# Performance work log

Measured on AMD Instinct MI355X. Metric: run time of the kernel, lower is better.

Reference implementation:

```python
import jax, jax.numpy as jnp
import numpy as np

D_MODEL = 2048
N_HEADS = 16
HEAD_DIM = 128
WINDOW = 512
ROPE_BASE = 10000.0
B, N = 2, 2048
INNER = N_HEADS * HEAD_DIM


def setup_inputs() -> dict:
    key = jax.random.key(0)
    k1, k2, k3 = jax.random.split(key, 3)
    x = jax.random.normal(k1, (B, N, D_MODEL), dtype=jnp.float32)
    # torch nn.Linear stores weight as [out_features, in_features]
    w_qkv = jax.random.normal(k2, (3 * INNER, D_MODEL), dtype=jnp.float32) / np.sqrt(D_MODEL)
    w_o = jax.random.normal(k3, (D_MODEL, INNER), dtype=jnp.float32) / np.sqrt(INNER)
    return {"x": x, "w_qkv": w_qkv, "w_o": w_o}


def _rotate_half(t):
    t1, t2 = jnp.split(t, 2, axis=-1)
    return jnp.concatenate([-t2, t1], axis=-1)


def _rope(q, k, offset=0):
    # q, k: [B, H, N, D]; GPT-NeoX half-split rotary embedding
    D = q.shape[-1]
    inv_freq = 1.0 / (ROPE_BASE ** (jnp.arange(0, D, 2, dtype=jnp.float32) / D))
    pos = jnp.arange(q.shape[2], dtype=jnp.float32) + offset
    ang = pos[:, None] * inv_freq[None, :]                 # [N, D/2]
    cos = jnp.concatenate([jnp.cos(ang), jnp.cos(ang)], axis=-1)  # [N, D]
    sin = jnp.concatenate([jnp.sin(ang), jnp.sin(ang)], axis=-1)
    q_r = q * cos + _rotate_half(q) * sin
    k_r = k * cos + _rotate_half(k) * sin
    return q_r, k_r


def reference(x, w_qkv, w_o):
    Bq, Nq, _ = x.shape
    # QKV projection (no bias)
    qkv = jnp.einsum('bnd,ed->bne', x, w_qkv)              # [B, N, 3*INNER]
    q, k, v = jnp.split(qkv, 3, axis=-1)
    def to_heads(t):
        return t.reshape(Bq, Nq, N_HEADS, HEAD_DIM).transpose(0, 2, 1, 3)  # [B,H,N,D]
    q, k, v = to_heads(q), to_heads(k), to_heads(v)
    q, k = _rope(q, k, offset=0)
    # sliding-window causal mask: valid key j for query i iff (i - WINDOW) < j <= i
    i = jnp.arange(Nq)[:, None]
    j = jnp.arange(Nq)[None, :]
    valid = (j > i - WINDOW) & (j <= i)                    # [N, N]
    scale = 1.0 / np.sqrt(HEAD_DIM)
    scores = jnp.einsum('bhnd,bhkd->bhnk', q, k) * scale   # [B,H,N,N]
    scores = jnp.where(valid[None, None], scores, -jnp.inf)
    att = jax.nn.softmax(scores, axis=-1)
    out = jnp.einsum('bhnk,bhkd->bhnd', att, v)
    out = out.transpose(0, 2, 1, 3).reshape(Bq, Nq, INNER)
    y = jnp.einsum('bni,di->bnd', out, w_o)
    return y
```

## Files before the change

kernel.cpp:

```cpp
#include <hip/hip_runtime.h>
#include <hip/hip_bf16.h>
#include <cstdint>

typedef __bf16 bf16x8 __attribute__((ext_vector_type(8)));
typedef float floatx4 __attribute__((ext_vector_type(4)));

__device__ __forceinline__ void gl2lds16(const void* g, void* l) {
  __builtin_amdgcn_global_load_lds(
      (const __attribute__((address_space(1))) unsigned int*)g,
      (__attribute__((address_space(3))) unsigned int*)(uintptr_t)l,
      16, 0, 0);
}

__global__ __launch_bounds__(256)
void cvt_kernel(const float* __restrict__ in, __hip_bfloat16* __restrict__ out, int n) {
  int i = (blockIdx.x * 256 + threadIdx.x) * 4;
  if (i >= n) return;
  const float4 v = *(const float4*)(in + i);
  out[i + 0] = __float2bfloat16(v.x);
  out[i + 1] = __float2bfloat16(v.y);
  out[i + 2] = __float2bfloat16(v.z);
  out[i + 3] = __float2bfloat16(v.w);
}

__global__ __launch_bounds__(256)
void gemm_bt(const __hip_bfloat16* __restrict__ A, const __hip_bfloat16* __restrict__ Bm,
             void* __restrict__ Cp, int M, int Nc, int K, int c_fp32)
{
  __shared__ __hip_bfloat16 As[128 * 32];
  __shared__ __hip_bfloat16 Bs[128 * 32];
  const int tid = threadIdx.x;
  const int lane = tid & 63, wave = tid >> 6;
  const int wm = (wave & 1) * 64, wn = (wave >> 1) * 64;
  const int m0 = blockIdx.x * 128, n0 = blockIdx.y * 128;
  const int lrow = lane & 15, lk = (lane >> 4) * 8;
  floatx4 acc[4][4] = {};
  const int c0 = tid, c1 = tid + 256;
  const int r0 = c0 >> 2, o0 = (c0 & 3) * 8;
  const int r1 = c1 >> 2, o1 = (c1 & 3) * 8;
  for (int kt = 0; kt < K; kt += 32) {
    __syncthreads();
    gl2lds16(A + (size_t)(m0 + r0) * K + kt + o0, &As[c0 * 8]);
    gl2lds16(A + (size_t)(m0 + r1) * K + kt + o1, &As[c1 * 8]);
    gl2lds16(Bm + (size_t)(n0 + r0) * K + kt + o0, &Bs[c0 * 8]);
    gl2lds16(Bm + (size_t)(n0 + r1) * K + kt + o1, &Bs[c1 * 8]);
    __syncthreads();
    bf16x8 af[4], bfr[4];
#pragma unroll
    for (int t = 0; t < 4; t++) af[t] = *(const bf16x8*)&As[(wm + t * 16 + lrow) * 32 + lk];
#pragma unroll
    for (int t = 0; t < 4; t++) bfr[t] = *(const bf16x8*)&Bs[(wn + t * 16 + lrow) * 32 + lk];
#pragma unroll
    for (int mt = 0; mt < 4; mt++)
#pragma unroll
      for (int nt = 0; nt < 4; nt++)
        acc[mt][nt] = __builtin_amdgcn_mfma_f32_16x16x32_bf16(af[mt], bfr[nt], acc[mt][nt], 0, 0, 0);
  }
  const int lq4 = (lane >> 4) * 4;
#pragma unroll
  for (int mt = 0; mt < 4; mt++)
#pragma unroll
    for (int nt = 0; nt < 4; nt++)
#pragma unroll
      for (int r = 0; r < 4; r++) {
        const int m = m0 + wm + mt * 16 + lq4 + r;
        const int n = n0 + wn + nt * 16 + lrow;
        const float v = acc[mt][nt][r];
        if (c_fp32) ((float*)Cp)[(size_t)m * Nc + n] = v;
        else ((__hip_bfloat16*)Cp)[(size_t)m * Nc + n] = __float2bfloat16(v);
      }
}

__global__ __launch_bounds__(256)
void gemm_qkv_fused(const __hip_bfloat16* __restrict__ A,
                    const __hip_bfloat16* __restrict__ W,
                    __hip_bfloat16* __restrict__ Qr,
                    __hip_bfloat16* __restrict__ Kr,
                    __hip_bfloat16* __restrict__ Vt)
{
  __shared__ alignas(16) char smem[16640];
  __shared__ float invf[64];
  __hip_bfloat16* As = (__hip_bfloat16*)smem;
  __hip_bfloat16* Bs = As + 128 * 32;
  __hip_bfloat16* Cs = (__hip_bfloat16*)smem;
  const int tid = threadIdx.x;
  if (tid < 64) invf[tid] = __expf(-(float)tid * 0.14391156831212787f);
  const int lane = tid & 63, wave = tid >> 6;
  const int wm = (wave & 1) * 64, wn = (wave >> 1) * 64;
  const int m0 = blockIdx.x * 128, n0 = blockIdx.y * 128;
  const int K = 2048;
  const int lrow = lane & 15, lk = (lane >> 4) * 8;
  floatx4 acc[4][4] = {};
  const int c0 = tid, c1 = tid + 256;
  const int r0 = c0 >> 2, o0 = (c0 & 3) * 8;
  const int r1 = c1 >> 2, o1 = (c1 & 3) * 8;
  for (int kt = 0; kt < K; kt += 32) {
    __syncthreads();
    gl2lds16(A + (size_t)(m0 + r0) * K + kt + o0, &As[c0 * 8]);
    gl2lds16(A + (size_t)(m0 + r1) * K + kt + o1, &As[c1 * 8]);
    gl2lds16(W + (size_t)(n0 + r0) * K + kt + o0, &Bs[c0 * 8]);
    gl2lds16(W + (size_t)(n0 + r1) * K + kt + o1, &Bs[c1 * 8]);
    __syncthreads();
    bf16x8 af[4], bfr[4];
#pragma unroll
    for (int t = 0; t < 4; t++) af[t] = *(const bf16x8*)&As[(wm + t * 16 + lrow) * 32 + lk];
#pragma unroll
    for (int t = 0; t < 4; t++) bfr[t] = *(const bf16x8*)&Bs[(wn + t * 16 + lrow) * 32 + lk];
#pragma unroll
    for (int mt = 0; mt < 4; mt++)
#pragma unroll
      for (int nt = 0; nt < 4; nt++)
        acc[mt][nt] = __builtin_amdgcn_mfma_f32_16x16x32_bf16(af[mt], bfr[nt], acc[mt][nt], 0, 0, 0);
  }
  const int lq4 = (lane >> 4) * 4;
  const int seg = n0 >> 11;
  const int h = (n0 & 2047) >> 7;
  const int b = m0 >> 11;
  const int bh = b * 16 + h;
  const int seq0 = m0 & 2047;
  const float qscale = (seg == 0) ? 0.08838834764831845f : 1.0f;
  for (int pass = 0; pass < 2; ++pass) {
    __syncthreads();
    if ((wave & 1) == pass) {
#pragma unroll
      for (int mt = 0; mt < 4; mt++)
#pragma unroll
        for (int nt = 0; nt < 4; nt++)
#pragma unroll
          for (int r = 0; r < 4; r++)
            Cs[(mt * 16 + lq4 + r) * 130 + wn + nt * 16 + lrow] =
                __float2bfloat16(acc[mt][nt][r]);
    }
    __syncthreads();
    if (seg < 2) {
      __hip_bfloat16* Out = seg ? Kr : Qr;
#pragma unroll
      for (int p = 0; p < 2; ++p) {
        const int row = (tid >> 3) + p * 32;
        const int oct = (tid & 7) * 8;
        const int m = m0 + pass * 64 + row;
        const float pos = (float)(m & 2047);
        alignas(16) __hip_bfloat16 lo[8], hi[8];
#pragma unroll
        for (int k2 = 0; k2 < 8; k2++) {
          const float ang = pos * invf[oct + k2];
          float sn, cs2;
          __sincosf(ang, &sn, &cs2);
          const float a  = __bfloat162float(Cs[row * 130 + oct + k2]);
          const float bb = __bfloat162float(Cs[row * 130 + oct + k2 + 64]);
          lo[k2] = __float2bfloat16((a * cs2 - bb * sn) * qscale);
          hi[k2] = __float2bfloat16((bb * cs2 + a * sn) * qscale);
        }
        const size_t ob = ((size_t)bh * 2048 + (size_t)(m & 2047)) * 128;
        *(bf16x8*)&Out[ob + oct]      = *(const bf16x8*)lo;
        *(bf16x8*)&Out[ob + oct + 64] = *(const bf16x8*)hi;
      }
    } else {
#pragma unroll
      for (int p = 0; p < 4; ++p) {
        const int d = (tid >> 3) + p * 32;
        const int s8 = (tid & 7) * 8;
        alignas(16) __hip_bfloat16 tmp[8];
#pragma unroll
        for (int k2 = 0; k2 < 8; k2++) tmp[k2] = Cs[(s8 + k2) * 130 + d];
        const size_t ob = ((size_t)bh * 128 + d) * 2048 + seq0 + pass * 64 + s8;
        *(bf16x8*)&Vt[ob] = *(const bf16x8*)tmp;
      }
    }
  }
}

__global__ __launch_bounds__(256)
void attn_swa(const __hip_bfloat16* __restrict__ Qr, const __hip_bfloat16* __restrict__ Kr,
              const __hip_bfloat16* __restrict__ Vt, __hip_bfloat16* __restrict__ Out)
{
  __shared__ __hip_bfloat16 Qs[64 * 128];
  __shared__ __hip_bfloat16 Ks[64 * 128];
  __shared__ __hip_bfloat16 Vs[128 * 64];
  __shared__ __hip_bfloat16 Pb[4][16 * 64];
  const int qt = blockIdx.x, bh = blockIdx.y;
  const int tid = threadIdx.x, lane = tid & 63, wave = tid >> 6;
  const int lrow = lane & 15, lk = (lane >> 4) * 8, lq4 = (lane >> 4) * 4;
  const int i0 = qt * 64;
  const float NEG_INF = -__builtin_inff();
  const __hip_bfloat16* Qh = Qr + (size_t)bh * 2048 * 128;
  const __hip_bfloat16* Kh = Kr + (size_t)bh * 2048 * 128;
  const __hip_bfloat16* Vh = Vt + (size_t)bh * 128 * 2048;
#pragma unroll
  for (int it = 0; it < 4; it++) {
    const int c = it * 256 + tid;
    gl2lds16(Qh + (size_t)(i0 + (c >> 4)) * 128 + (c & 15) * 8, &Qs[c * 8]);
  }
  floatx4 accO[8] = {};
  float m_i[4], l_i[4];
#pragma unroll
  for (int r = 0; r < 4; r++) { m_i[r] = NEG_INF; l_i[r] = 0.f; }
  const int lo = i0 - 511;
  const int jt_lo = (lo > 0 ? lo : 0) >> 6;
  const int jt_hi = i0 >> 6;
  const int imin = i0 + wave * 16;
  bf16x8 aq[4];
  for (int jt = jt_lo; jt <= jt_hi; jt++) {
    const int j0 = jt * 64;
    __syncthreads();
#pragma unroll
    for (int it = 0; it < 4; it++) {
      const int c = it * 256 + tid;
      gl2lds16(Kh + (size_t)(j0 + (c >> 4)) * 128 + (c & 15) * 8, &Ks[c * 8]);
      gl2lds16(Vh + (size_t)(c >> 3) * 2048 + j0 + (c & 7) * 8, &Vs[c * 8]);
    }
    __syncthreads();
    if (jt == jt_lo) {
#pragma unroll
      for (int ks = 0; ks < 4; ks++)
        aq[ks] = *(const bf16x8*)&Qs[(wave * 16 + lrow) * 128 + ks * 32 + lk];
    }
    floatx4 s[4] = {};
#pragma unroll
    for (int nt = 0; nt < 4; nt++)
#pragma unroll
      for (int ks = 0; ks < 4; ks++) {
        const bf16x8 bk = *(const bf16x8*)&Ks[(nt * 16 + lrow) * 128 + ks * 32 + lk];
        s[nt] = __builtin_amdgcn_mfma_f32_16x16x32_bf16(aq[ks], bk, s[nt], 0, 0, 0);
      }
    const bool full = (j0 + 63 <= imin) && (j0 >= imin + 15 - 511);
    float rmax[4];
#pragma unroll
    for (int r = 0; r < 4; r++) rmax[r] = NEG_INF;
    if (full) {
#pragma unroll
      for (int nt = 0; nt < 4; nt++)
#pragma unroll
        for (int r = 0; r < 4; r++) rmax[r] = fmaxf(rmax[r], s[nt][r]);
    } else {
#pragma unroll
      for (int nt = 0; nt < 4; nt++) {
        const int j = j0 + nt * 16 + lrow;
#pragma unroll
        for (int r = 0; r < 4; r++) {
          const int i = i0 + wave * 16 + lq4 + r;
          const float sv = ((j <= i) && (j > i - 512)) ? s[nt][r] : NEG_INF;
          s[nt][r] = sv;
          rmax[r] = fmaxf(rmax[r], sv);
        }
      }
    }
#pragma unroll
    for (int off = 1; off < 16; off <<= 1)
#pragma unroll
      for (int r = 0; r < 4; r++)
        rmax[r] = fmaxf(rmax[r], __shfl_xor(rmax[r], off, 16));
    float alpha[4], mnew[4];
#pragma unroll
    for (int r = 0; r < 4; r++) {
      mnew[r] = fmaxf(m_i[r], rmax[r]);
      alpha[r] = __expf(fminf(m_i[r] - mnew[r], 0.f));
      m_i[r] = mnew[r];
    }
    float rs[4] = {0.f, 0.f, 0.f, 0.f};
    if (full) {
#pragma unroll
      for (int nt = 0; nt < 4; nt++)
#pragma unroll
        for (int r = 0; r < 4; r++) {
          const float p = __expf(s[nt][r] - mnew[r]);
          s[nt][r] = p;
          rs[r] += p;
        }
    } else {
#pragma unroll
      for (int nt = 0; nt < 4; nt++)
#pragma unroll
        for (int r = 0; r < 4; r++) {
          const float sv = s[nt][r];
          const float p = (sv == NEG_INF) ? 0.f : __expf(sv - mnew[r]);
          s[nt][r] = p;
          rs[r] += p;
        }
    }
#pragma unroll
    for (int off = 1; off < 16; off <<= 1)
#pragma unroll
      for (int r = 0; r < 4; r++) rs[r] += __shfl_xor(rs[r], off, 16);
    floatx4 av;
#pragma unroll
    for (int r = 0; r < 4; r++) { l_i[r] = l_i[r] * alpha[r] + rs[r]; av[r] = alpha[r]; }
#pragma unroll
    for (int dt = 0; dt < 8; dt++) accO[dt] *= av;
#pragma unroll
    for (int nt = 0; nt < 4; nt++)
#pragma unroll
      for (int r = 0; r < 4; r++)
        Pb[wave][(lq4 + r) * 64 + nt * 16 + lrow] = __float2bfloat16(s[nt][r]);
    bf16x8 pa[2];
#pragma unroll
    for (int jf = 0; jf < 2; jf++)
      pa[jf] = *(const bf16x8*)&Pb[wave][lrow * 64 + jf * 32 + lk];
#pragma unroll
    for (int dt = 0; dt < 8; dt++)
#pragma unroll
      for (int jf = 0; jf < 2; jf++) {
        const bf16x8 bv = *(const bf16x8*)&Vs[(dt * 16 + lrow) * 64 + jf * 32 + lk];
        accO[dt] = __builtin_amdgcn_mfma_f32_16x16x32_bf16(pa[jf], bv, accO[dt], 0, 0, 0);
      }
  }
  const int b = bh >> 4, h = bh & 15;
#pragma unroll
  for (int dt = 0; dt < 8; dt++)
#pragma unroll
    for (int r = 0; r < 4; r++) {
      const int i = i0 + wave * 16 + lq4 + r;
      const int d = dt * 16 + lrow;
      Out[((size_t)(b * 2048 + i)) * 2048 + h * 128 + d] =
          __float2bfloat16(accO[dt][r] / l_i[r]);
    }
}

extern "C" void kernel_launch(void* const* d_in, const int* in_sizes, int n_in,
                              void* d_out, int out_size, void* d_ws, size_t ws_size,
                              hipStream_t stream)
{
  const float* x = (const float*)d_in[0];
  const float* w_qkv = (const float*)d_in[1];
  const float* w_o = (const float*)d_in[2];
  float* y = (float*)d_out;
  char* ws = (char*)d_ws;

  const size_t SZ_X = 16777216;
  const size_t SZ_WQKV = 25165824;
  const size_t SZ_Q = 16777216;

  __hip_bfloat16* xb = (__hip_bfloat16*)(ws);
  __hip_bfloat16* wqkvb = (__hip_bfloat16*)(ws + SZ_X);
  __hip_bfloat16* Qr = (__hip_bfloat16*)(ws + SZ_X + SZ_WQKV);
  __hip_bfloat16* Kr = (__hip_bfloat16*)(ws + SZ_X + SZ_WQKV + SZ_Q);
  __hip_bfloat16* Vt = (__hip_bfloat16*)(ws + SZ_X + SZ_WQKV + 2 * SZ_Q);

  cvt_kernel<<<dim3(8192), dim3(256), 0, stream>>>(x, xb, 8388608);
  cvt_kernel<<<dim3(12288), dim3(256), 0, stream>>>(w_qkv, wqkvb, 12582912);
  gemm_qkv_fused<<<dim3(32, 48), dim3(256), 0, stream>>>(xb, wqkvb, Qr, Kr, Vt);
  attn_swa<<<dim3(32, 32), dim3(256), 0, stream>>>(Qr, Kr, Vt, xb );
  cvt_kernel<<<dim3(4096), dim3(256), 0, stream>>>(w_o, wqkvb, 4194304);
  gemm_bt<<<dim3(32, 16), dim3(256), 0, stream>>>(xb, wqkvb, (void*)y, 4096, 2048, 2048, 1);
}
```

Measured before the change: 413.5 us.

## Use 128-query tiles with 8 waves and transposed MFMA operands in attention

The attention kernel now handles 128 queries per block with 512 threads, so each K/V tile loaded into LDS serves twice as many query rows. Q is staged through the K/V buffers, removing the dedicated Q buffer. The MFMA operands are swapped so that each lane owns a single query row. That makes the softmax reductions two cross-lane shuffles instead of four rounds over four rows, and lets P and the output be written as packed 64-bit stores. The P buffer is padded to a 72-element row stride. In exchange the grid has half as many blocks (512), and each block runs one extra K tile iteration that is partly masked.

```diff
diff --git a/kernel.cpp b/kernel.cpp
--- a/kernel.cpp
+++ b/kernel.cpp
@@ -170,102 +170,97 @@
   }
 }
 
-__global__ __launch_bounds__(256)
+__global__ __launch_bounds__(512)
 void attn_swa(const __hip_bfloat16* __restrict__ Qr, const __hip_bfloat16* __restrict__ Kr,
               const __hip_bfloat16* __restrict__ Vt, __hip_bfloat16* __restrict__ Out)
 {
-  __shared__ __hip_bfloat16 Qs[64 * 128];
   __shared__ __hip_bfloat16 Ks[64 * 128];
   __shared__ __hip_bfloat16 Vs[128 * 64];
-  __shared__ __hip_bfloat16 Pb[4][16 * 64];
+  __shared__ __hip_bfloat16 Pb[8][16 * 72];
   const int qt = blockIdx.x, bh = blockIdx.y;
   const int tid = threadIdx.x, lane = tid & 63, wave = tid >> 6;
   const int lrow = lane & 15, lk = (lane >> 4) * 8, lq4 = (lane >> 4) * 4;
-  const int i0 = qt * 64;
+  const int i0 = qt * 128;
   const float NEG_INF = -__builtin_inff();
   const __hip_bfloat16* Qh = Qr + (size_t)bh * 2048 * 128;
   const __hip_bfloat16* Kh = Kr + (size_t)bh * 2048 * 128;
   const __hip_bfloat16* Vh = Vt + (size_t)bh * 128 * 2048;
+
 #pragma unroll
   for (int it = 0; it < 4; it++) {
-    const int c = it * 256 + tid;
-    gl2lds16(Qh + (size_t)(i0 + (c >> 4)) * 128 + (c & 15) * 8, &Qs[c * 8]);
-  }
+    const int c = it * 512 + tid;
+    __hip_bfloat16* dst = (c < 1024) ? &Ks[c * 8] : &Vs[(c - 1024) * 8];
+    gl2lds16(Qh + (size_t)(i0 + (c >> 4)) * 128 + (c & 15) * 8, dst);
+  }
+  __syncthreads();
+  bf16x8 qf[4];
+  {
+    const __hip_bfloat16* qbuf = (wave < 4) ? Ks : Vs;
+    const int qrow = (wave & 3) * 16 + lrow;
+#pragma unroll
+    for (int ks = 0; ks < 4; ks++)
+      qf[ks] = *(const bf16x8*)&qbuf[qrow * 128 + ks * 32 + lk];
+  }
+
   floatx4 accO[8] = {};
-  float m_i[4], l_i[4];
-#pragma unroll
-  for (int r = 0; r < 4; r++) { m_i[r] = NEG_INF; l_i[r] = 0.f; }
+  float m_i = NEG_INF, l_i = 0.f;
+  const int iw = i0 + wave * 16 + lrow;
+  const int imin = i0 + wave * 16;
   const int lo = i0 - 511;
   const int jt_lo = (lo > 0 ? lo : 0) >> 6;
-  const int jt_hi = i0 >> 6;
-  const int imin = i0 + wave * 16;
-  bf16x8 aq[4];
+  const int jt_hi = (i0 + 127) >> 6;
+
   for (int jt = jt_lo; jt <= jt_hi; jt++) {
     const int j0 = jt * 64;
     __syncthreads();
 #pragma unroll
-    for (int it = 0; it < 4; it++) {
-      const int c = it * 256 + tid;
+    for (int it = 0; it < 2; it++) {
+      const int c = it * 512 + tid;
       gl2lds16(Kh + (size_t)(j0 + (c >> 4)) * 128 + (c & 15) * 8, &Ks[c * 8]);
       gl2lds16(Vh + (size_t)(c >> 3) * 2048 + j0 + (c & 7) * 8, &Vs[c * 8]);
     }
     __syncthreads();
-    if (jt == jt_lo) {
-#pragma unroll
-      for (int ks = 0; ks < 4; ks++)
-        aq[ks] = *(const bf16x8*)&Qs[(wave * 16 + lrow) * 128 + ks * 32 + lk];
-    }
     floatx4 s[4] = {};
 #pragma unroll
     for (int nt = 0; nt < 4; nt++)
 #pragma unroll
       for (int ks = 0; ks < 4; ks++) {
-        const bf16x8 bk = *(const bf16x8*)&Ks[(nt * 16 + lrow) * 128 + ks * 32 + lk];
-        s[nt] = __builtin_amdgcn_mfma_f32_16x16x32_bf16(aq[ks], bk, s[nt], 0, 0, 0);
+        const bf16x8 kf = *(const bf16x8*)&Ks[(nt * 16 + lrow) * 128 + ks * 32 + lk];
+        s[nt] = __builtin_amdgcn_mfma_f32_16x16x32_bf16(kf, qf[ks], s[nt], 0, 0, 0);
       }
     const bool full = (j0 + 63 <= imin) && (j0 >= imin + 15 - 511);
-    float rmax[4];
-#pragma unroll
-    for (int r = 0; r < 4; r++) rmax[r] = NEG_INF;
+    float rmax = NEG_INF;
     if (full) {
 #pragma unroll
       for (int nt = 0; nt < 4; nt++)
 #pragma unroll
-        for (int r = 0; r < 4; r++) rmax[r] = fmaxf(rmax[r], s[nt][r]);
+        for (int r = 0; r < 4; r++) rmax = fmaxf(rmax, s[nt][r]);
     } else {
 #pragma unroll
       for (int nt = 0; nt < 4; nt++) {
-        const int j = j0 + nt * 16 + lrow;
 #pragma unroll
         for (int r = 0; r < 4; r++) {
-          const int i = i0 + wave * 16 + lq4 + r;
-          const float sv = ((j <= i) && (j > i - 512)) ? s[nt][r] : NEG_INF;
+          const int j = j0 + nt * 16 + lq4 + r;
+          const float sv = ((j <= iw) && (j > iw - 512)) ? s[nt][r] : NEG_INF;
           s[nt][r] = sv;
-          rmax[r] = fmaxf(rmax[r], sv);
+          rmax = fmaxf(rmax, sv);
         }
       }
     }
-#pragma unroll
-    for (int off = 1; off < 16; off <<= 1)
-#pragma unroll
-      for (int r = 0; r < 4; r++)
-        rmax[r] = fmaxf(rmax[r], __shfl_xor(rmax[r], off, 16));
-    float alpha[4], mnew[4];
-#pragma unroll
-    for (int r = 0; r < 4; r++) {
-      mnew[r] = fmaxf(m_i[r], rmax[r]);
-      alpha[r] = __expf(fminf(m_i[r] - mnew[r], 0.f));
-      m_i[r] = mnew[r];
-    }
-    float rs[4] = {0.f, 0.f, 0.f, 0.f};
+    rmax = fmaxf(rmax, __shfl_xor(rmax, 16));
+    rmax = fmaxf(rmax, __shfl_xor(rmax, 32));
+    const float mnew = fmaxf(m_i, rmax);
+    const float alpha = __expf(fminf(m_i - mnew, 0.f));
+    m_i = mnew;
+    float rs = 0.f;
     if (full) {
 #pragma unroll
       for (int nt = 0; nt < 4; nt++)
 #pragma unroll
         for (int r = 0; r < 4; r++) {
-          const float p = __expf(s[nt][r] - mnew[r]);
+          const float p = __expf(s[nt][r] - mnew);
           s[nt][r] = p;
-          rs[r] += p;
+          rs += p;
         }
     } else {
 #pragma unroll
@@ -273,47 +268,45 @@
 #pragma unroll
         for (int r = 0; r < 4; r++) {
           const float sv = s[nt][r];
-          const float p = (sv == NEG_INF) ? 0.f : __expf(sv - mnew[r]);
+          const float p = (sv == NEG_INF) ? 0.f : __expf(sv - mnew);
           s[nt][r] = p;
-          rs[r] += p;
+          rs += p;
         }
     }
-#pragma unroll
-    for (int off = 1; off < 16; off <<= 1)
-#pragma unroll
-      for (int r = 0; r < 4; r++) rs[r] += __shfl_xor(rs[r], off, 16);
-    floatx4 av;
-#pragma unroll
-    for (int r = 0; r < 4; r++) { l_i[r] = l_i[r] * alpha[r] + rs[r]; av[r] = alpha[r]; }
-#pragma unroll
-    for (int dt = 0; dt < 8; dt++) accO[dt] *= av;
-#pragma unroll
-    for (int nt = 0; nt < 4; nt++)
-#pragma unroll
-      for (int r = 0; r < 4; r++)
-        Pb[wave][(lq4 + r) * 64 + nt * 16 + lrow] = __float2bfloat16(s[nt][r]);
-    bf16x8 pa[2];
+    rs += __shfl_xor(rs, 16);
+    rs += __shfl_xor(rs, 32);
+    l_i = l_i * alpha + rs;
+#pragma unroll
+    for (int dt = 0; dt < 8; dt++) accO[dt] *= alpha;
+#pragma unroll
+    for (int nt = 0; nt < 4; nt++) {
+      alignas(8) __hip_bfloat16 p4[4];
+#pragma unroll
+      for (int r = 0; r < 4; r++) p4[r] = __float2bfloat16(s[nt][r]);
+      *(uint64_t*)&Pb[wave][lrow * 72 + nt * 16 + lq4] = *(const uint64_t*)p4;
+    }
+    bf16x8 pf[2];
 #pragma unroll
     for (int jf = 0; jf < 2; jf++)
-      pa[jf] = *(const bf16x8*)&Pb[wave][lrow * 64 + jf * 32 + lk];
+      pf[jf] = *(const bf16x8*)&Pb[wave][lrow * 72 + jf * 32 + lk];
 #pragma unroll
     for (int dt = 0; dt < 8; dt++)
 #pragma unroll
       for (int jf = 0; jf < 2; jf++) {
-        const bf16x8 bv = *(const bf16x8*)&Vs[(dt * 16 + lrow) * 64 + jf * 32 + lk];
-        accO[dt] = __builtin_amdgcn_mfma_f32_16x16x32_bf16(pa[jf], bv, accO[dt], 0, 0, 0);
+        const bf16x8 vf = *(const bf16x8*)&Vs[(dt * 16 + lrow) * 64 + jf * 32 + lk];
+        accO[dt] = __builtin_amdgcn_mfma_f32_16x16x32_bf16(vf, pf[jf], accO[dt], 0, 0, 0);
       }
   }
   const int b = bh >> 4, h = bh & 15;
-#pragma unroll
-  for (int dt = 0; dt < 8; dt++)
-#pragma unroll
-    for (int r = 0; r < 4; r++) {
-      const int i = i0 + wave * 16 + lq4 + r;
-      const int d = dt * 16 + lrow;
-      Out[((size_t)(b * 2048 + i)) * 2048 + h * 128 + d] =
-          __float2bfloat16(accO[dt][r] / l_i[r]);
-    }
+  const float inv_l = 1.0f / l_i;
+  const size_t rowb = ((size_t)(b * 2048 + iw)) * 2048 + h * 128;
+#pragma unroll
+  for (int dt = 0; dt < 8; dt++) {
+    alignas(8) __hip_bfloat16 o4[4];
+#pragma unroll
+    for (int r = 0; r < 4; r++) o4[r] = __float2bfloat16(accO[dt][r] * inv_l);
+    *(uint64_t*)&Out[rowb + dt * 16 + lq4] = *(const uint64_t*)o4;
+  }
 }
 
 extern "C" void kernel_launch(void* const* d_in, const int* in_sizes, int n_in,
@@ -339,7 +332,7 @@
   cvt_kernel<<<dim3(8192), dim3(256), 0, stream>>>(x, xb, 8388608);
   cvt_kernel<<<dim3(12288), dim3(256), 0, stream>>>(w_qkv, wqkvb, 12582912);
   gemm_qkv_fused<<<dim3(32, 48), dim3(256), 0, stream>>>(xb, wqkvb, Qr, Kr, Vt);
-  attn_swa<<<dim3(32, 32), dim3(256), 0, stream>>>(Qr, Kr, Vt, xb );
+  attn_swa<<<dim3(16, 32), dim3(512), 0, stream>>>(Qr, Kr, Vt, xb );
   cvt_kernel<<<dim3(4096), dim3(256), 0, stream>>>(w_o, wqkvb, 4194304);
   gemm_bt<<<dim3(32, 16), dim3(256), 0, stream>>>(xb, wqkvb, (void*)y, 4096, 2048, 2048, 1);
 }
```

Measured after the change: 399.3 us. -3.5%, faster.
